# Performance work log

Hardware: AMD Instinct MI355X
Metric: run time of the kernel (lower is better)

The kernel has to match this reference:

```python
import jax, jax.numpy as jnp
import numpy as np

N_NODES = 50000


def sage_conv(x, src, dst, Wl, bl, Wr):
    # PyG SAGEConv (aggr='mean'): out_i = Wl @ mean_{j in N(i)} x_j + bl + Wr @ x_i
    msg = x[src]                                              # [E, d] gather
    agg = jax.ops.segment_sum(msg, dst, num_segments=N_NODES)  # [N, d]
    cnt = jax.ops.segment_sum(jnp.ones((src.shape[0],), x.dtype), dst,
                              num_segments=N_NODES)
    mean = agg / jnp.maximum(cnt, 1.0)[:, None]
    return mean @ Wl.T + bl + x @ Wr.T


def graph_forward(x, edge_index, W1l, b1, W1r, W2l, b2, W2r):
    src, dst = edge_index[0], edge_index[1]
    h = jnp.tanh(sage_conv(x, src, dst, W1l, b1, W1r))
    return jnp.tanh(sage_conv(h, src, dst, W2l, b2, W2r))


def setup_inputs() -> dict:
    key = jax.random.key(0)
    ks = jax.random.split(key, 16)
    E = 800000
    IN, HID, OUT = 128, 256, 128
    s = lambda fan: 1.0 / np.sqrt(fan)
    inp = {
        'x0': jax.random.normal(ks[0], (N_NODES, IN), jnp.float32),
        'x1': jax.random.normal(ks[1], (N_NODES, IN), jnp.float32),
        'edge_index0': jax.random.randint(ks[2], (2, E), 0, N_NODES),
        'edge_index1': jax.random.randint(ks[3], (2, E), 0, N_NODES),
    }
    for g, base in ((0, 4), (1, 10)):
        inp[f'W1l_{g}'] = jax.random.normal(ks[base + 0], (HID, IN), jnp.float32) * s(IN)
        inp[f'b1_{g}'] = jnp.zeros((HID,), jnp.float32)
        inp[f'W1r_{g}'] = jax.random.normal(ks[base + 1], (HID, IN), jnp.float32) * s(IN)
        inp[f'W2l_{g}'] = jax.random.normal(ks[base + 2], (OUT, HID), jnp.float32) * s(HID)
        inp[f'b2_{g}'] = jnp.zeros((OUT,), jnp.float32)
        inp[f'W2r_{g}'] = jax.random.normal(ks[base + 3], (OUT, HID), jnp.float32) * s(HID)
    return inp


def reference(x0, x1, edge_index0, edge_index1,
              W1l_0, b1_0, W1r_0, W2l_0, b2_0, W2r_0,
              W1l_1, b1_1, W1r_1, W2l_1, b2_1, W2r_1):
    out0 = graph_forward(x0, edge_index0, W1l_0, b1_0, W1r_0, W2l_0, b2_0, W2r_0)
    out1 = graph_forward(x1, edge_index1, W1l_1, b1_1, W1r_1, W2l_1, b2_1, W2r_1)
    return jnp.concatenate([out0, out1], axis=0)
```

## Files before the change

### kernel.cpp

```cpp
#include <hip/hip_runtime.h>
#include <cstddef>

#define N_NODES 50000
#define N_EDGES 800000
#define CAP 64
#define XU (N_NODES * 16)

typedef __attribute__((ext_vector_type(8))) _Float16 half8;
typedef __attribute__((ext_vector_type(2))) _Float16 half2v;
typedef __attribute__((ext_vector_type(4))) float f32x4;

__device__ __forceinline__ float fast_tanh(float x) {
    float t = __expf(2.0f * x);
    return 1.0f - 2.0f / (t + 1.0f);
}

#define XRNG ((N_NODES + 7) / 8)

__global__ __launch_bounds__(256) void prep_k(
        const int* __restrict__ src0, const int* __restrict__ dst0,
        const int* __restrict__ src1, const int* __restrict__ dst1,
        int* __restrict__ cnt, int* __restrict__ adj,
        const float* __restrict__ x0, const float* __restrict__ x1,
        const float* __restrict__ w00, const float* __restrict__ w01,
        const float* __restrict__ w02, const float* __restrict__ w03,
        const float* __restrict__ w10, const float* __restrict__ w11,
        const float* __restrict__ w12, const float* __restrict__ w13,
        _Float16* __restrict__ xd, _Float16* __restrict__ wd) {
    const int role = (blockIdx.x >> 3) & 1;
    const int idx8 = ((blockIdx.x >> 4) << 3) | (blockIdx.x & 7);
    if (role == 0) {
        const int g = idx8 >> 11;
        const int b = idx8 & 2047;
        const int* src = g ? src1 : src0;
        const int* dst = g ? dst1 : dst0;
        int* cg = cnt + g * N_NODES;
        int* ag = adj + (size_t)g * N_NODES * CAP;
        const int grp = b & 7;
        const int lo = grp * XRNG, hi = lo + XRNG;
        for (int e = (b >> 3) * 256 + threadIdx.x; e < N_EDGES; e += 65536) {
            int d = dst[e];
            if (d >= lo && d < hi) {
                int c = atomicAdd(&cg[d], 1);
                if (c < CAP) ag[d * CAP + c] = src[e];
            }
        }
    } else {
        const int total = 2 * XU + 32768;
        for (int i = idx8 * 256 + threadIdx.x; i < total; i += 4096 * 256) {
            const float* s; _Float16* d;
            if (i < 2 * XU) {
                int g = i >= XU ? 1 : 0;
                int l = i - g * XU;
                s = (g ? x1 : x0) + (size_t)l * 8;
                d = xd + (size_t)g * ((size_t)N_NODES * 256) + (size_t)l * 8;
            } else {
                int w = i - 2 * XU;
                int g = w >> 14, m = (w >> 12) & 3, l = w & 4095;
                const float* wm;
                if (g == 0) wm = (m == 0) ? w00 : (m == 1) ? w01 : (m == 2) ? w02 : w03;
                else        wm = (m == 0) ? w10 : (m == 1) ? w11 : (m == 2) ? w12 : w13;
                s = wm + (size_t)l * 8;
                d = wd + (size_t)g * 131072 + (size_t)m * 32768 + (size_t)l * 8;
            }
            float4 v0 = ((const float4*)s)[0], v1 = ((const float4*)s)[1];
            half8 o;
            o[0] = (_Float16)v0.x; o[1] = (_Float16)v0.y;
            o[2] = (_Float16)v0.z; o[3] = (_Float16)v0.w;
            o[4] = (_Float16)v1.x; o[5] = (_Float16)v1.y;
            o[6] = (_Float16)v1.z; o[7] = (_Float16)v1.w;
            *(half8*)d = o;
        }
    }
}

template <int OUTM, int RSU>
__global__ __launch_bounds__(256) void gather_mean_k(
        const unsigned* __restrict__ Xu, size_t xgs,
        const int* __restrict__ cnt, const int* __restrict__ adj,
        unsigned* __restrict__ outm, size_t ogs,
        const float* __restrict__ bias0, const float* __restrict__ bias1,
        float* __restrict__ outf, int N) {
    const int g = blockIdx.y;
    int gw = blockIdx.x * 4 + (threadIdx.x >> 6);
    if (gw >= N) return;
    const int lane = threadIdx.x & 63;
    const int deg0 = cnt[g * N_NODES + gw];
    const int deg = deg0 < CAP ? deg0 : CAP;
    const int* aj = adj + (size_t)g * N_NODES * CAP + (size_t)gw * CAP;
    const unsigned* Xl = Xu + (size_t)g * xgs + lane;
    float sx = 0.f, sy = 0.f;
    int n = 0;
    for (; n + 16 <= deg; n += 16) {
        unsigned u0  = Xl[(size_t)aj[n     ] * RSU];
        unsigned u1  = Xl[(size_t)aj[n +  1] * RSU];
        unsigned u2  = Xl[(size_t)aj[n +  2] * RSU];
        unsigned u3  = Xl[(size_t)aj[n +  3] * RSU];
        unsigned u4  = Xl[(size_t)aj[n +  4] * RSU];
        unsigned u5  = Xl[(size_t)aj[n +  5] * RSU];
        unsigned u6  = Xl[(size_t)aj[n +  6] * RSU];
        unsigned u7  = Xl[(size_t)aj[n +  7] * RSU];
        unsigned u8  = Xl[(size_t)aj[n +  8] * RSU];
        unsigned u9  = Xl[(size_t)aj[n +  9] * RSU];
        unsigned u10 = Xl[(size_t)aj[n + 10] * RSU];
        unsigned u11 = Xl[(size_t)aj[n + 11] * RSU];
        unsigned u12 = Xl[(size_t)aj[n + 12] * RSU];
        unsigned u13 = Xl[(size_t)aj[n + 13] * RSU];
        unsigned u14 = Xl[(size_t)aj[n + 14] * RSU];
        unsigned u15 = Xl[(size_t)aj[n + 15] * RSU];
        half2v h0  = __builtin_bit_cast(half2v, u0);
        half2v h1  = __builtin_bit_cast(half2v, u1);
        half2v h2  = __builtin_bit_cast(half2v, u2);
        half2v h3  = __builtin_bit_cast(half2v, u3);
        half2v h4  = __builtin_bit_cast(half2v, u4);
        half2v h5  = __builtin_bit_cast(half2v, u5);
        half2v h6  = __builtin_bit_cast(half2v, u6);
        half2v h7  = __builtin_bit_cast(half2v, u7);
        half2v h8  = __builtin_bit_cast(half2v, u8);
        half2v h9  = __builtin_bit_cast(half2v, u9);
        half2v h10 = __builtin_bit_cast(half2v, u10);
        half2v h11 = __builtin_bit_cast(half2v, u11);
        half2v h12 = __builtin_bit_cast(half2v, u12);
        half2v h13 = __builtin_bit_cast(half2v, u13);
        half2v h14 = __builtin_bit_cast(half2v, u14);
        half2v h15 = __builtin_bit_cast(half2v, u15);
        sx += (float)h0.x + (float)h1.x + (float)h2.x + (float)h3.x
            + (float)h4.x + (float)h5.x + (float)h6.x + (float)h7.x
            + (float)h8.x + (float)h9.x + (float)h10.x + (float)h11.x
            + (float)h12.x + (float)h13.x + (float)h14.x + (float)h15.x;
        sy += (float)h0.y + (float)h1.y + (float)h2.y + (float)h3.y
            + (float)h4.y + (float)h5.y + (float)h6.y + (float)h7.y
            + (float)h8.y + (float)h9.y + (float)h10.y + (float)h11.y
            + (float)h12.y + (float)h13.y + (float)h14.y + (float)h15.y;
    }
    for (; n + 4 <= deg; n += 4) {
        unsigned u0 = Xl[(size_t)aj[n    ] * RSU];
        unsigned u1 = Xl[(size_t)aj[n + 1] * RSU];
        unsigned u2 = Xl[(size_t)aj[n + 2] * RSU];
        unsigned u3 = Xl[(size_t)aj[n + 3] * RSU];
        half2v h0 = __builtin_bit_cast(half2v, u0);
        half2v h1 = __builtin_bit_cast(half2v, u1);
        half2v h2 = __builtin_bit_cast(half2v, u2);
        half2v h3 = __builtin_bit_cast(half2v, u3);
        sx += (float)h0.x + (float)h1.x + (float)h2.x + (float)h3.x;
        sy += (float)h0.y + (float)h1.y + (float)h2.y + (float)h3.y;
    }
    for (; n < deg; n++) {
        unsigned u = Xl[(size_t)aj[n] * RSU];
        half2v h = __builtin_bit_cast(half2v, u);
        sx += (float)h.x;
        sy += (float)h.y;
    }
    float inv = 1.0f / (float)(deg0 > 0 ? deg0 : 1);
    float mx = sx * inv, my = sy * inv;
    if (OUTM == 0) {
        half2v o;
        o.x = (_Float16)mx; o.y = (_Float16)my;
        outm[(size_t)g * ogs + (size_t)gw * 64 + lane] =
            __builtin_bit_cast(unsigned, o);
    } else {
        unsigned pu = Xu[(size_t)g * xgs + (size_t)gw * 128 + 64 + lane];
        half2v ph = __builtin_bit_cast(half2v, pu);
        const float* bias = g ? bias1 : bias0;
        float2 bb = ((const float2*)bias)[lane];
        float2 o;
        o.x = fast_tanh(mx + (float)ph.x + bb.x);
        o.y = fast_tanh(my + (float)ph.y + bb.y);
        ((float2*)(outf + (size_t)g * N_NODES * 128))[(size_t)gw * 64 + lane] = o;
    }
}

#define TM 128
#define TN 64
#define TK 32
#define LSTR 40
#define OSTR 72
#define SMEM_BYTES (TM * OSTR * 2)

template <bool TANH>
__global__ __launch_bounds__(256)
void gemm_f16_k(const _Float16* __restrict__ A1, const _Float16* __restrict__ B1, int K1,
                const _Float16* __restrict__ A2, const _Float16* __restrict__ B2, int K2,
                const float* __restrict__ bias,
                _Float16* __restrict__ outh, int N, int Md) {
    __shared__ char smem[SMEM_BYTES];
    _Float16 (*sA)[LSTR] = reinterpret_cast<_Float16(*)[LSTR]>(smem);
    _Float16 (*sB)[LSTR] = reinterpret_cast<_Float16(*)[LSTR]>(smem + TM * LSTR * 2);
    _Float16 (*sO)[OSTR] = reinterpret_cast<_Float16(*)[OSTR]>(smem);

    const int tid = threadIdx.x;
    const int lane = tid & 63;
    const int wave = tid >> 6;
    const int waveM = (wave & 1) * 64;
    const int waveN = (wave >> 1) * 32;
    const int rowBase = blockIdx.y * TM;
    const int colBase = blockIdx.x * TN;
    const int Ktot = K1 + K2;

    const int r0 = tid >> 2, c0 = tid & 3;
    const int r1 = r0 + 64;
    const int gr0 = rowBase + r0, gr1 = rowBase + r1;

    f32x4 acc[4][2] = {};
    half8 pA0, pA1, pB0;

    auto load_tile = [&](int k0) {
        const _Float16 *A, *B; int ko, ld;
        if (k0 < K1) { A = A1; B = B1; ko = k0;      ld = K1; }
        else         { A = A2; B = B2; ko = k0 - K1; ld = K2; }
        half8 z = {(_Float16)0, (_Float16)0, (_Float16)0, (_Float16)0,
                   (_Float16)0, (_Float16)0, (_Float16)0, (_Float16)0};
        size_t a0 = (size_t)gr0 * ld + ko + c0 * 8;
        size_t a1 = (size_t)gr1 * ld + ko + c0 * 8;
        pA0 = gr0 < N ? *(const half8*)(A + a0) : z;
        pA1 = gr1 < N ? *(const half8*)(A + a1) : z;
        pB0 = *(const half8*)(B + (size_t)(colBase + r0) * ld + ko + c0 * 8);
    };
    auto store_tile = [&]() {
        *(half8*)&sA[r0][c0 * 8] = pA0;
        *(half8*)&sA[r1][c0 * 8] = pA1;
        *(half8*)&sB[r0][c0 * 8] = pB0;
    };

    const int fm = lane & 15;
    const int fq = (lane >> 4) * 8;
    half8 fa[4], fb[2];
    auto read_frags = [&]() {
        #pragma unroll
        for (int mi = 0; mi < 4; mi++)
            fa[mi] = *(const half8*)&sA[waveM + mi * 16 + fm][fq];
        #pragma unroll
        for (int ni = 0; ni < 2; ni++)
            fb[ni] = *(const half8*)&sB[waveN + ni * 16 + fm][fq];
    };
    auto mfma_all = [&]() {
        #pragma unroll
        for (int mi = 0; mi < 4; mi++)
            #pragma unroll
            for (int ni = 0; ni < 2; ni++)
                acc[mi][ni] = __builtin_amdgcn_mfma_f32_16x16x32_f16(
                    fa[mi], fb[ni], acc[mi][ni], 0, 0, 0);
    };

    load_tile(0);
    store_tile();
    __syncthreads();

    for (int k0 = TK; k0 < Ktot; k0 += TK) {
        read_frags();
        load_tile(k0);
        mfma_all();
        __syncthreads();
        store_tile();
        __syncthreads();
    }
    read_frags();
    mfma_all();

    __syncthreads();
    {
        const int lr0 = waveM + (lane >> 4) * 4;
        const int lc0 = waveN + fm;
        #pragma unroll
        for (int ni = 0; ni < 2; ni++) {
            float bv = bias ? bias[colBase + lc0 + ni * 16] : 0.0f;
            #pragma unroll
            for (int mi = 0; mi < 4; mi++)
                #pragma unroll
                for (int r = 0; r < 4; r++) {
                    float v = acc[mi][ni][r] + bv;
                    if (TANH) v = fast_tanh(v);
                    sO[lr0 + mi * 16 + r][lc0 + ni * 16] = (_Float16)v;
                }
        }
    }
    __syncthreads();
    {
        const int rr = tid >> 3;
        const int cc = (tid & 7) * 8;
        #pragma unroll
        for (int p = 0; p < 4; p++) {
            int row = p * 32 + rr;
            int grow = rowBase + row;
            if (grow < N)
                *(half8*)(outh + (size_t)grow * Md + colBase + cc) =
                    *(const half8*)&sO[row][cc];
        }
    }
}

extern "C" void kernel_launch(void* const* d_in, const int* in_sizes, int n_in,
                              void* d_out, int out_size, void* d_ws, size_t ws_size,
                              hipStream_t stream) {
    const int N = N_NODES, E = N_EDGES;

    const float* x[2]   = {(const float*)d_in[0],  (const float*)d_in[1]};
    const int*   ei[2]  = {(const int*)d_in[2],    (const int*)d_in[3]};
    const float* W1l[2] = {(const float*)d_in[4],  (const float*)d_in[10]};
    const float* b1[2]  = {(const float*)d_in[5],  (const float*)d_in[11]};
    const float* W1r[2] = {(const float*)d_in[6],  (const float*)d_in[12]};
    const float* W2l[2] = {(const float*)d_in[7],  (const float*)d_in[13]};
    const float* b2[2]  = {(const float*)d_in[8],  (const float*)d_in[14]};
    const float* W2r[2] = {(const float*)d_in[9],  (const float*)d_in[15]};
    float* out = (float*)d_out;

    char* wsb = (char*)d_ws;
    const size_t MiB = 1u << 20;
    int*      cnt  = (int*)(wsb);
    int*      adj  = (int*)(wsb + 1 * MiB);
    _Float16* Wh   = (_Float16*)(wsb + 27 * MiB);
    _Float16* feat = (_Float16*)(wsb + 28 * MiB);
    _Float16* h16  = (_Float16*)(wsb + 80 * MiB);

    const size_t FGS = (size_t)N * 256;
    const size_t WGS = 131072;

    const int gemm_rows = (N + TM - 1) / TM;
    const int agg_x = N / 4;

    (void)hipMemsetAsync(cnt, 0, 2 * (size_t)N * sizeof(int), stream);
    prep_k<<<8192, 256, 0, stream>>>(
        ei[0], ei[0] + E, ei[1], ei[1] + E, cnt, adj,
        x[0], x[1],
        W1l[0], W1r[0], W2l[0], W2r[0],
        W1l[1], W1r[1], W2l[1], W2r[1],
        feat, Wh);

    gather_mean_k<0, 64><<<dim3(agg_x, 2), 256, 0, stream>>>(
        (const unsigned*)feat, FGS / 2, cnt, adj,
        (unsigned*)(feat + (size_t)N * 128), FGS / 2,
        nullptr, nullptr, nullptr, N);

    for (int g = 0; g < 2; g++) {
        _Float16* x16g   = feat + g * FGS;
        _Float16* mean16 = x16g + (size_t)N * 128;
        _Float16* hz16   = x16g;
        _Float16* W1l16  = Wh + g * WGS;
        _Float16* W1r16  = W1l16 + 32768;
        _Float16* W2cat  = W1l16 + 65536;
        gemm_f16_k<true><<<dim3(4, gemm_rows), 256, 0, stream>>>(
            mean16, W1l16, 128, x16g, W1r16, 128, b1[g], h16, N, 256);
        gemm_f16_k<false><<<dim3(4, gemm_rows), 256, 0, stream>>>(
            h16, W2cat, 256, nullptr, nullptr, 0, nullptr, hz16, N, 256);
    }

    gather_mean_k<1, 128><<<dim3(agg_x, 2), 256, 0, stream>>>(
        (const unsigned*)feat, FGS / 2, cnt, adj,
        nullptr, 0, b2[0], b2[1], out, N);
}
```

Baseline: 430.6 us.

## Partition edges by destination range before adjacency fill to avoid redundant edge scans

The old prep kernel had each of 8 destination-range groups scan all edges and keep only those in its range, so the edge list was read eight times. The new code first bins each edge into one of 8 destination partitions, using shared-memory counts per block and one global atomic per partition, and writes (src,dst) pairs into per-partition buffers. A second kernel then fills the per-node adjacency lists from each partition's pairs, keeping the locality of the atomics. The cost is an extra launch and an extra write and read of the pair buffer, which reuses workspace later taken by h16. Fixed PCAP capacities could overflow on skewed inputs.

Measured after the change: 519.7 us. 1.21x slower.

```diff
diff --git a/kernel.cpp b/kernel.cpp
--- a/kernel.cpp
+++ b/kernel.cpp
@@ -5,6 +5,8 @@
 #define N_EDGES 800000
 #define CAP 64
 #define XU (N_NODES * 16)
+#define XRNG ((N_NODES + 7) / 8)
+#define PCAP 131072
 
 typedef __attribute__((ext_vector_type(8))) _Float16 half8;
 typedef __attribute__((ext_vector_type(2))) _Float16 half2v;
@@ -15,62 +17,86 @@
     return 1.0f - 2.0f / (t + 1.0f);
 }
 
-#define XRNG ((N_NODES + 7) / 8)
-
-__global__ __launch_bounds__(256) void prep_k(
+__global__ __launch_bounds__(256) void part_convert_k(
         const int* __restrict__ src0, const int* __restrict__ dst0,
         const int* __restrict__ src1, const int* __restrict__ dst1,
-        int* __restrict__ cnt, int* __restrict__ adj,
+        int* __restrict__ pcnt, int2* __restrict__ pairs,
         const float* __restrict__ x0, const float* __restrict__ x1,
         const float* __restrict__ w00, const float* __restrict__ w01,
         const float* __restrict__ w02, const float* __restrict__ w03,
         const float* __restrict__ w10, const float* __restrict__ w11,
         const float* __restrict__ w12, const float* __restrict__ w13,
         _Float16* __restrict__ xd, _Float16* __restrict__ wd) {
-    const int role = (blockIdx.x >> 3) & 1;
-    const int idx8 = ((blockIdx.x >> 4) << 3) | (blockIdx.x & 7);
+    const int bi = blockIdx.x;
+    int role, idx;
+    if (bi < 12500) { role = bi & 1; idx = bi >> 1; }
+    else            { role = 1;      idx = 6250 + (bi - 12500); }
+
     if (role == 0) {
-        const int g = idx8 >> 11;
-        const int b = idx8 & 2047;
-        const int* src = g ? src1 : src0;
-        const int* dst = g ? dst1 : dst0;
-        int* cg = cnt + g * N_NODES;
-        int* ag = adj + (size_t)g * N_NODES * CAP;
-        const int grp = b & 7;
-        const int lo = grp * XRNG, hi = lo + XRNG;
-        for (int e = (b >> 3) * 256 + threadIdx.x; e < N_EDGES; e += 65536) {
-            int d = dst[e];
-            if (d >= lo && d < hi) {
-                int c = atomicAdd(&cg[d], 1);
-                if (c < CAP) ag[d * CAP + c] = src[e];
-            }
+        __shared__ int hcnt[8], hbase[8];
+        const int g = idx >= 3125 ? 1 : 0;
+        const int b = idx - g * 3125;
+        const int e = b * 256 + threadIdx.x;
+        const int sv = (g ? src1 : src0)[e];
+        const int dv = (g ? dst1 : dst0)[e];
+        const int key = dv / XRNG;
+        if (threadIdx.x < 8) hcnt[threadIdx.x] = 0;
+        __syncthreads();
+        int rank = atomicAdd(&hcnt[key], 1);
+        __syncthreads();
+        if (threadIdx.x < 8) {
+            int c = hcnt[threadIdx.x];
+            hbase[threadIdx.x] =
+                c ? atomicAdd(&pcnt[(g * 8 + threadIdx.x) * 16], c) : 0;
         }
+        __syncthreads();
+        int2 pr; pr.x = sv; pr.y = dv;
+        pairs[(size_t)(g * 8 + key) * PCAP + hbase[key] + rank] = pr;
     } else {
-        const int total = 2 * XU + 32768;
-        for (int i = idx8 * 256 + threadIdx.x; i < total; i += 4096 * 256) {
-            const float* s; _Float16* d;
-            if (i < 2 * XU) {
-                int g = i >= XU ? 1 : 0;
-                int l = i - g * XU;
-                s = (g ? x1 : x0) + (size_t)l * 8;
-                d = xd + (size_t)g * ((size_t)N_NODES * 256) + (size_t)l * 8;
-            } else {
-                int w = i - 2 * XU;
-                int g = w >> 14, m = (w >> 12) & 3, l = w & 4095;
-                const float* wm;
-                if (g == 0) wm = (m == 0) ? w00 : (m == 1) ? w01 : (m == 2) ? w02 : w03;
-                else        wm = (m == 0) ? w10 : (m == 1) ? w11 : (m == 2) ? w12 : w13;
-                s = wm + (size_t)l * 8;
-                d = wd + (size_t)g * 131072 + (size_t)m * 32768 + (size_t)l * 8;
-            }
-            float4 v0 = ((const float4*)s)[0], v1 = ((const float4*)s)[1];
-            half8 o;
-            o[0] = (_Float16)v0.x; o[1] = (_Float16)v0.y;
-            o[2] = (_Float16)v0.z; o[3] = (_Float16)v0.w;
-            o[4] = (_Float16)v1.x; o[5] = (_Float16)v1.y;
-            o[6] = (_Float16)v1.z; o[7] = (_Float16)v1.w;
-            *(half8*)d = o;
+        int i = idx * 256 + threadIdx.x;
+        if (i >= 2 * XU + 32768) return;
+        const float* s; _Float16* d;
+        if (i < 2 * XU) {
+            int g = i >= XU ? 1 : 0;
+            int l = i - g * XU;
+            s = (g ? x1 : x0) + (size_t)l * 8;
+            d = xd + (size_t)g * ((size_t)N_NODES * 256) + (size_t)l * 8;
+        } else {
+            int w = i - 2 * XU;
+            int g = w >> 14, m = (w >> 12) & 3, l = w & 4095;
+            const float* wm;
+            if (g == 0) wm = (m == 0) ? w00 : (m == 1) ? w01 : (m == 2) ? w02 : w03;
+            else        wm = (m == 0) ? w10 : (m == 1) ? w11 : (m == 2) ? w12 : w13;
+            s = wm + (size_t)l * 8;
+            d = wd + (size_t)g * 131072 + (size_t)m * 32768 + (size_t)l * 8;
         }
+        float4 v0 = ((const float4*)s)[0], v1 = ((const float4*)s)[1];
+        half8 o;
+        o[0] = (_Float16)v0.x; o[1] = (_Float16)v0.y;
+        o[2] = (_Float16)v0.z; o[3] = (_Float16)v0.w;
+        o[4] = (_Float16)v1.x; o[5] = (_Float16)v1.y;
+        o[6] = (_Float16)v1.z; o[7] = (_Float16)v1.w;
+        *(half8*)d = o;
+    }
+}
+
+__global__ __launch_bounds__(256) void fill_k(const int* __restrict__ pcnt,
+                                              const int2* __restrict__ pairs,
+                                              int* __restrict__ cnt,
+                                              int* __restrict__ adj) {
+    const int g = blockIdx.x >> 11;
+    const int b = blockIdx.x & 2047;
+    const int grp = b & 7;
+    const int pidx = g * 8 + grp;
+    int m = pcnt[pidx * 16];
+    m = m < PCAP ? m : PCAP;
+    const int2* pp = pairs + (size_t)pidx * PCAP;
+    int* cg = cnt + g * N_NODES;
+    int* ag = adj + (size_t)g * N_NODES * CAP;
+    for (int j = (b >> 3) * 256 + threadIdx.x; j < m; j += 65536) {
+        int2 pr = pp[j];
+        int c = atomicAdd(&cg[pr.y], 1);
+        if (c < CAP) ag[pr.y * CAP + c] = pr.x;
     }
 }
 
@@ -306,11 +332,13 @@
 
     char* wsb = (char*)d_ws;
     const size_t MiB = 1u << 20;
-    int*      cnt  = (int*)(wsb);
-    int*      adj  = (int*)(wsb + 1 * MiB);
-    _Float16* Wh   = (_Float16*)(wsb + 27 * MiB);
-    _Float16* feat = (_Float16*)(wsb + 28 * MiB);
-    _Float16* h16  = (_Float16*)(wsb + 80 * MiB);
+    int*      cnt   = (int*)(wsb);
+    int*      pcnt  = (int*)(wsb + 400000);
+    int*      adj   = (int*)(wsb + 1 * MiB);
+    _Float16* Wh    = (_Float16*)(wsb + 27 * MiB);
+    _Float16* feat  = (_Float16*)(wsb + 28 * MiB);
+    int2*     pairs = (int2*)(wsb + 80 * MiB);
+    _Float16* h16   = (_Float16*)(wsb + 80 * MiB);
 
     const size_t FGS = (size_t)N * 256;
     const size_t WGS = 131072;
@@ -318,13 +346,14 @@
     const int gemm_rows = (N + TM - 1) / TM;
     const int agg_x = N / 4;
 
-    (void)hipMemsetAsync(cnt, 0, 2 * (size_t)N * sizeof(int), stream);
-    prep_k<<<8192, 256, 0, stream>>>(
-        ei[0], ei[0] + E, ei[1], ei[1] + E, cnt, adj,
+    (void)hipMemsetAsync(cnt, 0, 400000 + 1024, stream);
+    part_convert_k<<<12628, 256, 0, stream>>>(
+        ei[0], ei[0] + E, ei[1], ei[1] + E, pcnt, pairs,
         x[0], x[1],
         W1l[0], W1r[0], W2l[0], W2r[0],
         W1l[1], W1r[1], W2l[1], W2r[1],
         feat, Wh);
+    fill_k<<<4096, 256, 0, stream>>>(pcnt, pairs, cnt, adj);
 
     gather_mean_k<0, 64><<<dim3(agg_x, 2), 256, 0, stream>>>(
         (const unsigned*)feat, FGS / 2, cnt, adj,
```
